# Performance work log

Measured on AMD Instinct MI355X. Metric: run time of the kernel, lower is better.

## Reference

```python
import jax, jax.numpy as jnp
import numpy as np

N = 4096; E = 32768; S = 64; V = 16; H0 = 64; H1 = 16; STEPS = 3
SQRT3 = float(np.sqrt(3.0))


def _tp(sx, vx, sy, vy):
    # full CG tensor product restricted to paths landing in 0e/1o
    # sx [n,m0], vx [n,m1,3], sy [n,k0], vy [n,k1,3]
    n = sx.shape[0]
    ss = (sx[:, :, None] * sy[:, None, :]).reshape(n, -1)              # 0e x 0e -> 0e
    dd = (jnp.einsum('nmi,nki->nmk', vx, vy) / SQRT3).reshape(n, -1)    # 1o . 1o -> 0e
    sv = (sx[:, :, None, None] * vy[:, None, :, :]).reshape(n, -1, 3)   # 0e x 1o -> 1o
    vs = (vx[:, :, None, :] * sy[:, None, :, None]).reshape(n, -1, 3)   # 1o x 0e -> 1o
    return jnp.concatenate([ss, dd], -1), jnp.concatenate([sv, vs], -2)


def _tpl_gate(sx, vx, sy, vy, ws, b, wv, n0):
    # TensorProductLinearGate: tensor_product -> Linear -> gate
    s_tp, v_tp = _tp(sx, vx, sy, vy)
    s = s_tp @ ws + b                                  # scalars + gate scalars
    v = jnp.einsum('ntd,tm->nmd', v_tp, wv)
    scal = jax.nn.gelu(s[:, :n0])
    gates = jax.nn.sigmoid(s[:, n0:])
    return scal, v * gates[:, :, None]


def _seg_mean(x, idx, n):
    s = jax.ops.segment_sum(x, idx, num_segments=n)
    c = jax.ops.segment_sum(jnp.ones((x.shape[0],), x.dtype), idx, num_segments=n)
    c = jnp.maximum(c, 1.0).reshape((n,) + (1,) * (x.ndim - 1))
    return s / c


def setup_inputs() -> dict:
    key = jax.random.key(0)
    ks = jax.random.split(key, 20)
    f32 = jnp.float32

    def w(k, shape):
        return jax.random.normal(k, shape, f32) / np.sqrt(shape[-2]).astype(np.float32)

    def bias(k, shape):
        return 0.1 * jax.random.normal(k, shape, f32)

    E1 = 2 * (S + V)          # 160: edge block0 TP width
    E2 = H0 + H1              # 80: edge blocks 1-2 TP width
    K0 = H0 + 1; K1 = H1 + 1  # message concat sh
    N0TP = S * K0 + V * K1    # 4432
    N1TP = S * K1 + V * K0    # 2128
    return {
        'node_s': jax.random.normal(ks[0], (N, S), f32),
        'node_v': jax.random.normal(ks[1], (N, V, 3), f32),
        'senders': jax.random.randint(ks[2], (E,), 0, N, jnp.int32),
        'receivers': jax.random.randint(ks[3], (E,), 0, N, jnp.int32),
        'e1_ws': w(ks[4], (STEPS, E1, H0 + H1)),
        'e1_b': bias(ks[5], (STEPS, H0 + H1)),
        'e1_wv': w(ks[6], (STEPS, E1, H1)),
        'e2_ws': w(ks[7], (STEPS, 2, E2, H0 + H1)),
        'e2_b': bias(ks[8], (STEPS, 2, H0 + H1)),
        'e2_wv': w(ks[9], (STEPS, 2, E2, H1)),
        'n_ws': w(ks[10], (STEPS, 3, N0TP, S + V)),
        'n_b': bias(ks[11], (STEPS, 3, S + V)),
        'n_wv': w(ks[12], (STEPS, 3, N1TP, V)),
        'l_ws': w(ks[13], (STEPS, S, S)),
        'l_b': bias(ks[14], (STEPS, S)),
        'l_wv': w(ks[15], (STEPS, V, V)),
    }


def reference(node_s, node_v, senders, receivers, e1_ws, e1_b, e1_wv,
              e2_ws, e2_b, e2_wv, n_ws, n_b, n_wv, l_ws, l_b, l_wv):
    norm = float(E - 1)
    for step in range(STEPS):
        s_i, v_i = node_s[senders], node_v[senders]
        s_j, v_j = node_s[receivers], node_v[receivers]
        r = v_i[:, 0] - v_j[:, 0]                    # slice_by_mul[:1] = positions
        rn = jnp.linalg.norm(r, axis=-1, keepdims=True)
        unit = r / jnp.maximum(rn, 1e-9)
        a_s = jnp.ones((E, 1), node_s.dtype)          # Y_0, component norm
        a_v = (SQRT3 * unit)[:, None, :]              # Y_1, component norm
        m_s = jnp.concatenate([s_i, s_j], -1)
        m_v = jnp.concatenate([v_i, v_j], -2)
        for blk in range(3):
            if blk == 0:
                ws, b, wv = e1_ws[step], e1_b[step], e1_wv[step]
            else:
                ws, b, wv = e2_ws[step, blk - 1], e2_b[step, blk - 1], e2_wv[step, blk - 1]
            m_s, m_v = _tpl_gate(m_s, m_v, a_s, a_v, ws, b, wv, H0)
        # ---- aggregate (segment_mean) + normalize_messages ----
        ms = _seg_mean(m_s, receivers, N) / norm
        mv = _seg_mean(m_v, receivers, N) / norm
        as_ = _seg_mean(a_s, receivers, N) / norm
        av = _seg_mean(a_v, receivers, N) / norm
        y_s = jnp.concatenate([ms, as_], -1)          # [N, H0+1]
        y_v = jnp.concatenate([mv, av], -2)           # [N, H1+1, 3]
        for blk in range(3):
            node_s, node_v = _tpl_gate(node_s, node_v, y_s, y_v,
                                       n_ws[step, blk], n_b[step, blk], n_wv[step, blk], S)
        # ---- final per-step Linear(irreps_in) ----
        node_s = node_s @ l_ws[step] + l_b[step]
        node_v = jnp.einsum('nmd,mk->nkd', node_v, l_wv[step])
    return jnp.concatenate([node_v.reshape(node_v.shape[0], -1), node_s], -1)
```

## Files before the change

### kernel.cpp

```cpp
#include <hip/hip_runtime.h>
#include <math.h>

constexpr int NND = 4096;
constexpr int EDG = 32768;
constexpr float SQRT3  = 1.7320508075688772f;
constexpr float ISQRT3 = 0.5773502691896258f;
constexpr float NORMI  = 1.0f / 32767.0f;

__device__ __forceinline__ float gelu_f(float x) {
    float x3 = x * x * x;
    return 0.5f * x * (1.0f + tanhf(0.7978845608028654f * (x + 0.044715f * x3)));
}
__device__ __forceinline__ float sigmoid_f(float x) {
    return 1.0f / (1.0f + expf(-x));
}

template<int NO4>
__device__ __forceinline__ void rank1(float* acc, float x, const float* w) {
#pragma unroll
    for (int u = 0; u < NO4; ++u) {
        const float4 q = *reinterpret_cast<const float4*>(w + 4 * u);
        acc[4*u+0] = fmaf(x, q.x, acc[4*u+0]);
        acc[4*u+1] = fmaf(x, q.y, acc[4*u+1]);
        acc[4*u+2] = fmaf(x, q.z, acc[4*u+2]);
        acc[4*u+3] = fmaf(x, q.w, acc[4*u+3]);
    }
}

__global__ __launch_bounds__(256)
void segnn_deg_kernel(const int* __restrict__ rcv, int* __restrict__ deg) {
    const int e = blockIdx.x * 256 + threadIdx.x;
    if (e < EDG) atomicAdd(deg + rcv[e], 1);
}

__global__ __launch_bounds__(1024)
void segnn_scan_kernel(const int* __restrict__ deg, int* __restrict__ off) {
    __shared__ int tots[1024];
    const int t = threadIdx.x;
    const int v0 = deg[4*t], v1 = deg[4*t+1], v2 = deg[4*t+2], v3 = deg[4*t+3];
    const int p1 = v0, p2 = p1 + v1, p3 = p2 + v2, p4 = p3 + v3;
    tots[t] = p4;
    __syncthreads();
    for (int d = 1; d < 1024; d <<= 1) {
        const int add = (t >= d) ? tots[t - d] : 0;
        __syncthreads();
        tots[t] += add;
        __syncthreads();
    }
    const int excl = t ? tots[t-1] : 0;
    off[4*t+0] = excl;
    off[4*t+1] = excl + p1;
    off[4*t+2] = excl + p2;
    off[4*t+3] = excl + p3;
    if (t == 1023) off[4096] = tots[1023];
}

__global__ __launch_bounds__(256)
void segnn_scatter_kernel(const int* __restrict__ rcv, const int* __restrict__ off,
                          int* __restrict__ cursor, int* __restrict__ elist) {
    const int e = blockIdx.x * 256 + threadIdx.x;
    if (e < EDG) {
        const int j = rcv[e];
        const int p = atomicAdd(cursor + j, 1);
        elist[off[j] + p] = e;
    }
}

template<int NSX, int NVX>
__device__ __forceinline__ void edge_gemm_phase(
    const int tid,
    const float* __restrict__ Ws, const float* __restrict__ Bs,
    const float* __restrict__ Wv,
    const float (*XT)[20], const float (*X2T)[20],
    float (*red)[16][8][6], float (*Cbuf)[96], float (*Cv)[48])
{
    const int cs   = tid & 15;
    const int rgl  = (tid >> 4) & 3;
    const int wvw  = tid >> 6;
    const int eg   = wvw & 1;
    const int kh   = wvw >> 1;
    const int lane = tid & 63;
    constexpr int KA = NSX + NVX;
    constexpr int CH = KA / 8;

    {
        float acc[8][6];
#pragma unroll
        for (int j = 0; j < 8; ++j)
#pragma unroll
            for (int c = 0; c < 6; ++c) acc[j][c] = 0.0f;
        const int r0 = (kh*4 + rgl) * CH;
#pragma unroll 2
        for (int rr = 0; rr < CH; ++rr) {
            const int r = r0 + rr;
            const float* wp = Ws + r*80 + cs;
            const float w0 = wp[0], w1 = wp[16], w2 = wp[32], w3 = wp[48], w4 = wp[64];
            const float w5 = (r < NSX) ? Wv[r*16 + cs] : 0.0f;
            const float4 xa = *reinterpret_cast<const float4*>(&XT[r][8*eg]);
            const float4 xb = *reinterpret_cast<const float4*>(&XT[r][8*eg+4]);
            const float xe[8] = { xa.x,xa.y,xa.z,xa.w, xb.x,xb.y,xb.z,xb.w };
#pragma unroll
            for (int j = 0; j < 8; ++j) {
                acc[j][0] = fmaf(xe[j], w0, acc[j][0]);
                acc[j][1] = fmaf(xe[j], w1, acc[j][1]);
                acc[j][2] = fmaf(xe[j], w2, acc[j][2]);
                acc[j][3] = fmaf(xe[j], w3, acc[j][3]);
                acc[j][4] = fmaf(xe[j], w4, acc[j][4]);
                acc[j][5] = fmaf(xe[j], w5, acc[j][5]);
            }
        }
#pragma unroll
        for (int j = 0; j < 8; ++j)
#pragma unroll
            for (int c = 0; c < 6; ++c) {
                float a = acc[j][c];
                a += __shfl_xor(a, 16);
                a += __shfl_xor(a, 32);
                acc[j][c] = a;
            }
        if (lane < 16) {
#pragma unroll
            for (int j = 0; j < 8; ++j)
#pragma unroll
                for (int c = 0; c < 6; ++c) red[wvw][lane][j][c] = acc[j][c];
        }
    }
    __syncthreads();
    for (int idx = tid; idx < 16*96; idx += 256) {
        const int e = idx / 96, col = idx - e*96;
        const int eg2 = e >> 3, j = e & 7;
        const int cs2 = col & 15, ci = col >> 4;
        float s = red[eg2][cs2][j][ci] + red[2+eg2][cs2][j][ci];
        if (col < 80) s += Bs[col];
        Cbuf[e][col] = s;
    }
    __syncthreads();

    {
        constexpr int CHB = NVX / 8;
        float av[8][3];
#pragma unroll
        for (int j = 0; j < 8; ++j) { av[j][0]=0.0f; av[j][1]=0.0f; av[j][2]=0.0f; }
        const int m0 = (kh*4 + rgl) * CHB;
#pragma unroll
        for (int mm = 0; mm < CHB; ++mm) {
            const int m = m0 + mm;
            const float w = Wv[(NSX + m)*16 + cs];
#pragma unroll
            for (int d = 0; d < 3; ++d) {
                const float4 xa = *reinterpret_cast<const float4*>(&X2T[d*NVX + m][8*eg]);
                const float4 xb = *reinterpret_cast<const float4*>(&X2T[d*NVX + m][8*eg+4]);
                const float xe[8] = { xa.x,xa.y,xa.z,xa.w, xb.x,xb.y,xb.z,xb.w };
#pragma unroll
                for (int j = 0; j < 8; ++j) av[j][d] = fmaf(xe[j], w, av[j][d]);
            }
        }
#pragma unroll
        for (int j = 0; j < 8; ++j)
#pragma unroll
            for (int d = 0; d < 3; ++d) {
                float a = av[j][d];
                a += __shfl_xor(a, 16);
                a += __shfl_xor(a, 32);
                av[j][d] = a;
            }
        if (lane < 16) {
#pragma unroll
            for (int j = 0; j < 8; ++j)
#pragma unroll
                for (int d = 0; d < 3; ++d) red[wvw][lane][j][d] = av[j][d];
        }
    }
    __syncthreads();
    for (int idx = tid; idx < 16*48; idx += 256) {
        const int e = idx / 48, q = idx - e*48;
        const int o = q / 3, d = q - 3*o;
        const int eg2 = e >> 3, j = e & 7;
        Cv[e][q] = red[eg2][o][j][d] + red[2+eg2][o][j][d];
    }
    __syncthreads();
}

__global__ __launch_bounds__(256, 3)
void segnn_edge_fused(const float* __restrict__ cs, const float* __restrict__ cv,
                      const int* __restrict__ snd, const int* __restrict__ rcv,
                      const float* __restrict__ W0s, const float* __restrict__ B0, const float* __restrict__ W0v,
                      const float* __restrict__ W1s, const float* __restrict__ B1, const float* __restrict__ W1v,
                      const float* __restrict__ W2s, const float* __restrict__ B2, const float* __restrict__ W2v,
                      float* __restrict__ msg) {
    __shared__ __align__(16) float XT[160][20];
    __shared__ __align__(16) float X2T[96][20];
    __shared__ float red[4][16][8][6];
    __shared__ float Cbuf[16][96];
    __shared__ float Cv[16][48];
    __shared__ float uu[16][4];
    __shared__ int   nd[16][2];

    const int tid = threadIdx.x;
    const int e0  = blockIdx.x * 16;

    if (tid < 16) { nd[tid][0] = snd[e0+tid]; nd[tid][1] = rcv[e0+tid]; }
    __syncthreads();
    for (int idx = tid; idx < 16*128; idx += 256) {
        const int e = idx >> 7, m = idx & 127;
        const int node = nd[e][m >> 6];
        XT[m][e] = cs[(size_t)node*64 + (m & 63)];
    }
    for (int idx = tid; idx < 16*96; idx += 256) {
        const int e = idx / 96, q = idx - e*96;
        const int part = q / 48, md = q - part*48;
        const int m = md / 3, d = md - m*3;
        const int node = nd[e][part];
        X2T[d*32 + part*16 + m][e] = cv[(size_t)node*48 + m*3 + d];
    }
    __syncthreads();
    if (tid < 16) {
        const float rx = X2T[0][tid]  - X2T[16][tid];
        const float ry = X2T[32][tid] - X2T[48][tid];
        const float rz = X2T[64][tid] - X2T[80][tid];
        const float rinv = 1.0f / fmaxf(sqrtf(rx*rx+ry*ry+rz*rz), 1e-9f);
        uu[tid][0] = rx*rinv; uu[tid][1] = ry*rinv; uu[tid][2] = rz*rinv;
    }
    __syncthreads();
    for (int idx = tid; idx < 16*32; idx += 256) {
        const int e = idx >> 5, mm = idx & 31;
        XT[128 + mm][e] = X2T[mm][e]*uu[e][0] + X2T[32+mm][e]*uu[e][1] + X2T[64+mm][e]*uu[e][2];
    }
    __syncthreads();

    edge_gemm_phase<128,32>(tid, W0s, B0, W0v, XT, X2T, red, Cbuf, Cv);
    for (int idx = tid; idx < 16*64; idx += 256) {
        const int e = idx >> 6, m = idx & 63;
        XT[m][e] = gelu_f(Cbuf[e][m]);
    }
    for (int idx = tid; idx < 16*16; idx += 256) {
        const int e = idx >> 4, o = idx & 15;
        const float g = sigmoid_f(Cbuf[e][64+o]);
        const float t = Cbuf[e][80+o] * SQRT3;
        float p = 0.0f;
#pragma unroll
        for (int d = 0; d < 3; ++d) {
            const float vd = fmaf(t, uu[e][d], Cv[e][o*3+d]) * g;
            X2T[d*16 + o][e] = vd;
            p = fmaf(vd, uu[e][d], p);
        }
        XT[64 + o][e] = p;
    }
    __syncthreads();

    edge_gemm_phase<64,16>(tid, W1s, B1, W1v, XT, X2T, red, Cbuf, Cv);
    for (int idx = tid; idx < 16*64; idx += 256) {
        const int e = idx >> 6, m = idx & 63;
        XT[m][e] = gelu_f(Cbuf[e][m]);
    }
    for (int idx = tid; idx < 16*16; idx += 256) {
        const int e = idx >> 4, o = idx & 15;
        const float g = sigmoid_f(Cbuf[e][64+o]);
        const float t = Cbuf[e][80+o] * SQRT3;
        float p = 0.0f;
#pragma unroll
        for (int d = 0; d < 3; ++d) {
            const float vd = fmaf(t, uu[e][d], Cv[e][o*3+d]) * g;
            X2T[d*16 + o][e] = vd;
            p = fmaf(vd, uu[e][d], p);
        }
        XT[64 + o][e] = p;
    }
    __syncthreads();

    edge_gemm_phase<64,16>(tid, W2s, B2, W2v, XT, X2T, red, Cbuf, Cv);
    for (int idx = tid; idx < 16*115; idx += 256) {
        const int e = idx / 115, f = idx - e*115;
        float vv;
        if (f < 64) {
            vv = gelu_f(Cbuf[e][f]);
        } else if (f < 112) {
            const int q = f - 64, o = q / 3, d = q - 3*o;
            const float g = sigmoid_f(Cbuf[e][64+o]);
            vv = fmaf(Cbuf[e][80+o] * SQRT3, uu[e][d], Cv[e][q]) * g;
        } else {
            vv = uu[e][f-112];
        }
        msg[(size_t)(e0+e)*116 + f] = vv;
    }
}

__global__ __launch_bounds__(128)
void segnn_gather_kernel(const float* __restrict__ msg, const int* __restrict__ off,
                         const int* __restrict__ elist,
                         float* __restrict__ y_s, float* __restrict__ y_v) {
    const int n = blockIdx.x, f = threadIdx.x;
    const int o0 = off[n], o1 = off[n+1];
    const int deg = o1 - o0;
    float acc = 0.0f;
    for (int p = o0; p < o1; ++p) {
        const int eid = elist[p];
        if (f < 115) acc += msg[(size_t)eid*116 + f];
    }
    const float inv = NORMI / (float)(deg > 0 ? deg : 1);
    if (f < 64)        y_s[(size_t)n*65 + f] = acc * inv;
    else if (f < 112)  y_v[(size_t)n*51 + (f-64)] = acc * inv;
    else if (f < 115)  y_v[(size_t)n*51 + 48 + (f-112)] = SQRT3 * acc * inv;
    else if (f == 115) y_s[(size_t)n*65 + 64] = deg ? NORMI : 0.0f;
}

__global__ __launch_bounds__(512, 4)
void segnn_node_kernel(const float* __restrict__ in_s, const float* __restrict__ in_v,
                       const float* __restrict__ y_s, const float* __restrict__ y_v,
                       const float* __restrict__ W,  const float* __restrict__ B,
                       const float* __restrict__ Wv,
                       float* __restrict__ out_s, float* __restrict__ out_v) {
    __shared__ __align__(16) float xsL[8*65];
    __shared__ __align__(16) float ysL[8*65];
    __shared__ __align__(16) float xvL[8*49];
    __shared__ __align__(16) float yvL[8*51];
    __shared__ __align__(16) float Xa[2][3072];
    __shared__ __align__(16) float red[8][16][40];
    __shared__ float finGG[8*16];

    const int tid  = threadIdx.x;
    const int lane = tid & 63;
    const int wv   = tid >> 6;
    const int nb0  = blockIdx.x * 8;

    for (int idx = tid; idx < 8*64; idx += 512) { const int n = idx >> 6, m = idx & 63; xsL[n*65+m] = in_s[(size_t)(nb0+n)*64 + m]; }
    for (int idx = tid; idx < 8*65; idx += 512) { const int n = idx / 65, k = idx - n*65; ysL[n*65+k] = y_s[(size_t)(nb0+n)*65 + k]; }
    for (int idx = tid; idx < 8*48; idx += 512) { const int n = idx / 48, m = idx - n*48; xvL[n*49+m] = in_v[(size_t)(nb0+n)*48 + m]; }
    for (int idx = tid; idx < 8*51; idx += 512) { const int n = idx / 51, m = idx - n*51; yvL[n*51+m] = y_v[(size_t)(nb0+n)*51 + m]; }
    __syncthreads();

    {
        const int cs = tid & 15;
        const int rowgrp = tid >> 4;

        float acc[8][5];
#pragma unroll
        for (int n = 0; n < 8; ++n)
#pragma unroll
            for (int c = 0; c < 5; ++c) acc[n][c] = 0.0f;

        auto genS = [&](int t, int b) {
            const int base = t * 128;
#pragma unroll
            for (int ii = 0; ii < 2; ++ii) {
                const int idx = tid + ii*512;
                const int rl = idx >> 3, n = idx & 7;
                const int r = base + rl;
                float val = 0.0f;
                if (r < 4160) {
                    const int m = r / 65, k = r - m*65;
                    val = xsL[n*65+m] * ysL[n*65+k];
                } else if (r < 4432) {
                    const int q = r - 4160;
                    const int m = q / 17, k = q - m*17;
                    val = (xvL[n*49+m*3+0]*yvL[n*51+k*3+0] +
                           xvL[n*49+m*3+1]*yvL[n*51+k*3+1] +
                           xvL[n*49+m*3+2]*yvL[n*51+k*3+2]) * ISQRT3;
                }
                Xa[b][idx] = val;
            }
        };

        genS(0, 0);
        __syncthreads();
        for (int t = 0; t < 35; ++t) {
            if (t + 1 < 35) genS(t + 1, (t + 1) & 1);
            const int base = t * 128;
            const float* Xb = &Xa[t & 1][0];
#pragma unroll
            for (int vv = 0; vv < 4; ++vv) {
                const int rl = rowgrp + 32*vv;
                const int r  = base + rl;
                const int wr = r < 4431 ? r : 4431;
                const float* wp = W + (size_t)wr * 80 + cs;
                const float w0 = wp[0], w1 = wp[16], w2 = wp[32], w3 = wp[48], w4_ = wp[64];
                const float4 xq0 = *reinterpret_cast<const float4*>(&Xb[rl*8]);
                const float4 xq1 = *reinterpret_cast<const float4*>(&Xb[rl*8+4]);
                const float xn[8] = { xq0.x, xq0.y, xq0.z, xq0.w, xq1.x, xq1.y, xq1.z, xq1.w };
#pragma unroll
                for (int n = 0; n < 8; ++n) {
                    acc[n][0] = fmaf(xn[n], w0,  acc[n][0]);
                    acc[n][1] = fmaf(xn[n], w1,  acc[n][1]);
                    acc[n][2] = fmaf(xn[n], w2,  acc[n][2]);
                    acc[n][3] = fmaf(xn[n], w3,  acc[n][3]);
                    acc[n][4] = fmaf(xn[n], w4_, acc[n][4]);
                }
            }
            __syncthreads();
        }

#pragma unroll
        for (int n = 0; n < 8; ++n)
#pragma unroll
            for (int c = 0; c < 5; ++c) {
                float a = acc[n][c];
                a += __shfl_xor(a, 16);
                a += __shfl_xor(a, 32);
                if (lane < 16) red[wv][lane][n*5+c] = a;
            }
        __syncthreads();
        for (int idx = tid; idx < 8*80; idx += 512) {
            const int n = idx / 80, col = idx - n*80;
            const int cs2 = col & 15, ci2 = col >> 4;
            float s = B[col];
#pragma unroll
            for (int w = 0; w < 8; ++w) s += red[w][cs2][n*5+ci2];
            if (col < 64) out_s[(size_t)(nb0+n)*64 + col] = gelu_f(s);
            else          finGG[n*16 + (col-64)] = s;
        }
    }

    {
        const int j4 = tid & 3;
        const int ngrp = (tid >> 2) & 1;
        const int rg = tid >> 3;

        float av[12][4];
#pragma unroll
        for (int a = 0; a < 12; ++a)
#pragma unroll
            for (int c = 0; c < 4; ++c) av[a][c] = 0.0f;

        auto genV = [&](int t, int b) {
            const int base = t * 128;
#pragma unroll
            for (int ii = 0; ii < 6; ++ii) {
                const int idx = tid + ii*512;
                const int rl = idx / 24, ar = idx - rl*24;
                const int n = ar / 3, d = ar - n*3;
                const int r = base + rl;
                float val = 0.0f;
                if (r < 1088) {
                    const int m = r / 17, k = r - m*17;
                    val = xsL[n*65+m] * yvL[n*51+k*3+d];
                } else if (r < 2128) {
                    const int q = r - 1088;
                    const int m = q / 65, k = q - m*65;
                    val = xvL[n*49+m*3+d] * ysL[n*65+k];
                }
                Xa[b][idx] = val;
            }
        };

        genV(0, 0);
        __syncthreads();
        for (int t = 0; t < 17; ++t) {
            if (t + 1 < 17) genV(t + 1, (t + 1) & 1);
            const int base = t * 128;
            const float* Xb = &Xa[t & 1][0];
#pragma unroll
            for (int vv = 0; vv < 2; ++vv) {
                const int rl = rg + 64*vv;
                const int r  = base + rl;
                const int wr = r < 2127 ? r : 2127;
                const float4 w4 = *reinterpret_cast<const float4*>(&Wv[(size_t)wr*16 + 4*j4]);
                const float4 xq0 = *reinterpret_cast<const float4*>(&Xb[rl*24 + 12*ngrp]);
                const float4 xq1 = *reinterpret_cast<const float4*>(&Xb[rl*24 + 12*ngrp + 4]);
                const float4 xq2 = *reinterpret_cast<const float4*>(&Xb[rl*24 + 12*ngrp + 8]);
                const float xr[12] = { xq0.x,xq0.y,xq0.z,xq0.w, xq1.x,xq1.y,xq1.z,xq1.w, xq2.x,xq2.y,xq2.z,xq2.w };
#pragma unroll
                for (int a = 0; a < 12; ++a) {
                    av[a][0] = fmaf(xr[a], w4.x, av[a][0]);
                    av[a][1] = fmaf(xr[a], w4.y, av[a][1]);
                    av[a][2] = fmaf(xr[a], w4.z, av[a][2]);
                    av[a][3] = fmaf(xr[a], w4.w, av[a][3]);
                }
            }
            __syncthreads();
        }

        float* redf = &red[0][0][0];
#pragma unroll
        for (int a = 0; a < 12; ++a)
#pragma unroll
            for (int c = 0; c < 4; ++c) {
                float x = av[a][c];
                x += __shfl_xor(x, 8);
                x += __shfl_xor(x, 16);
                x += __shfl_xor(x, 32);
                if (lane < 8) redf[wv*384 + lane*48 + a*4 + c] = x;
            }
        __syncthreads();
        for (int idx = tid; idx < 24*16; idx += 512) {
            const int ar = idx >> 4, j = idx & 15;
            const int n = ar / 3, d = ar - n*3;
            const int ng2 = ar / 12, a2 = ar - 12*ng2;
            const int jj4 = j >> 2, c2 = j & 3;
            float s = 0.0f;
#pragma unroll
            for (int w = 0; w < 8; ++w) s += redf[w*384 + (jj4 + 4*ng2)*48 + a2*4 + c2];
            out_v[(size_t)(nb0+n)*48 + j*3 + d] = s * sigmoid_f(finGG[n*16 + j]);
        }
    }
}

__global__ __launch_bounds__(256)
void segnn_linear_kernel(const float* __restrict__ in_s, const float* __restrict__ in_v,
                         const float* __restrict__ lws, const float* __restrict__ lb,
                         const float* __restrict__ lwv,
                         float* __restrict__ out_s, float* __restrict__ out_v,
                         float* __restrict__ out_cat) {
    const int idx = blockIdx.x * 256 + threadIdx.x;
    if (idx >= NND * 112) return;
    const int nidx = idx / 112, f = idx - nidx * 112;
    if (f < 48) {
        const int k = f / 3, d = f - 3*k;
        const float* vp = in_v + (size_t)nidx * 48 + d;
        float acc = 0.0f;
#pragma unroll
        for (int m = 0; m < 16; ++m) acc = fmaf(vp[m*3], lwv[m*16 + k], acc);
        if (out_cat) out_cat[(size_t)nidx*112 + f] = acc;
        else         out_v[(size_t)nidx*48 + f] = acc;
    } else {
        const int o = f - 48;
        const float* sp = in_s + (size_t)nidx * 64;
        float acc = lb[o];
#pragma unroll
        for (int m = 0; m < 64; ++m) acc = fmaf(sp[m], lws[m*64 + o], acc);
        if (out_cat) out_cat[(size_t)nidx*112 + f] = acc;
        else         out_s[(size_t)nidx*64 + o] = acc;
    }
}

extern "C" void kernel_launch(void* const* d_in, const int* in_sizes, int n_in,
                              void* d_out, int out_size, void* d_ws, size_t ws_size,
                              hipStream_t stream) {
    const float* in_s  = (const float*)d_in[0];
    const float* in_v  = (const float*)d_in[1];
    const int*   snd   = (const int*)  d_in[2];
    const int*   rcv   = (const int*)  d_in[3];
    const float* e1_ws = (const float*)d_in[4];
    const float* e1_b  = (const float*)d_in[5];
    const float* e1_wv = (const float*)d_in[6];
    const float* e2_ws = (const float*)d_in[7];
    const float* e2_b  = (const float*)d_in[8];
    const float* e2_wv = (const float*)d_in[9];
    const float* n_ws  = (const float*)d_in[10];
    const float* n_b   = (const float*)d_in[11];
    const float* n_wv  = (const float*)d_in[12];
    const float* l_ws  = (const float*)d_in[13];
    const float* l_b   = (const float*)d_in[14];
    const float* l_wv  = (const float*)d_in[15];

    float* ws    = (float*)d_ws;
    float* cur_s = ws;
    float* cur_v = cur_s + 262144;
    float* nxt_s = cur_v + 196608;
    float* nxt_v = nxt_s + 262144;
    float* y_s   = nxt_v + 196608;
    float* y_v   = y_s + 266240;
    float* msg   = y_v + 208896;
    int*   deg    = (int*)(msg + 3801088);
    int*   cursor = deg + 4096;
    int*   off    = cursor + 4096;
    int*   elist  = off + 4097;

    hipMemsetAsync(deg, 0, (size_t)8192 * sizeof(int), stream);
    hipMemcpyAsync(cur_s, in_s, (size_t)262144 * sizeof(float), hipMemcpyDeviceToDevice, stream);
    hipMemcpyAsync(cur_v, in_v, (size_t)196608 * sizeof(float), hipMemcpyDeviceToDevice, stream);
    segnn_deg_kernel<<<EDG/256, 256, 0, stream>>>(rcv, deg);
    segnn_scan_kernel<<<1, 1024, 0, stream>>>(deg, off);
    segnn_scatter_kernel<<<EDG/256, 256, 0, stream>>>(rcv, off, cursor, elist);

    for (int step = 0; step < 3; ++step) {
        segnn_edge_fused<<<EDG/16, 256, 0, stream>>>(cur_s, cur_v, snd, rcv,
            e1_ws + (size_t)step*160*80, e1_b + step*80, e1_wv + (size_t)step*160*16,
            e2_ws + (size_t)(step*2+0)*80*80, e2_b + (step*2+0)*80, e2_wv + (size_t)(step*2+0)*80*16,
            e2_ws + (size_t)(step*2+1)*80*80, e2_b + (step*2+1)*80, e2_wv + (size_t)(step*2+1)*80*16,
            msg);
        segnn_gather_kernel<<<NND, 128, 0, stream>>>(msg, off, elist, y_s, y_v);

        segnn_node_kernel<<<NND/8, 512, 0, stream>>>(cur_s, cur_v, y_s, y_v,
            n_ws + (size_t)(step*3+0)*4432*80, n_b + (step*3+0)*80, n_wv + (size_t)(step*3+0)*2128*16,
            nxt_s, nxt_v);
        segnn_node_kernel<<<NND/8, 512, 0, stream>>>(nxt_s, nxt_v, y_s, y_v,
            n_ws + (size_t)(step*3+1)*4432*80, n_b + (step*3+1)*80, n_wv + (size_t)(step*3+1)*2128*16,
            cur_s, cur_v);
        segnn_node_kernel<<<NND/8, 512, 0, stream>>>(cur_s, cur_v, y_s, y_v,
            n_ws + (size_t)(step*3+2)*4432*80, n_b + (step*3+2)*80, n_wv + (size_t)(step*3+2)*2128*16,
            nxt_s, nxt_v);

        segnn_linear_kernel<<<(NND*112 + 255)/256, 256, 0, stream>>>(nxt_s, nxt_v,
            l_ws + (size_t)step*64*64, l_b + step*64, l_wv + (size_t)step*16*16,
            cur_s, cur_v, (step == 2) ? (float*)d_out : nullptr);
    }
}
```

Measured before the change: 1.181 ms.

## Make edge kernel warp-independent and prefetch node-kernel weights into registers

The edge kernel now gives each 64-lane wave its own 8 edges with private shared buffers. Partial sums are reduced with shuffles and written directly, which removes the block-wide reduction buffers and most __syncthreads; each block handles 32 edges. The node kernel prefetches the next tile's weights into registers alongside the shared-memory generation and uses raw s_barrier with an lgkmcnt wait. Reduction buffers are padded against bank conflicts. Occupancy hints drop from 3 and 4 blocks per SM to 2, trading occupancy for register headroom, and the wave-private path relies on compiler barriers alone for ordering within a wave.

```diff
diff --git a/kernel.cpp b/kernel.cpp
--- a/kernel.cpp
+++ b/kernel.cpp
@@ -13,18 +13,6 @@
 }
 __device__ __forceinline__ float sigmoid_f(float x) {
     return 1.0f / (1.0f + expf(-x));
-}
-
-template<int NO4>
-__device__ __forceinline__ void rank1(float* acc, float x, const float* w) {
-#pragma unroll
-    for (int u = 0; u < NO4; ++u) {
-        const float4 q = *reinterpret_cast<const float4*>(w + 4 * u);
-        acc[4*u+0] = fmaf(x, q.x, acc[4*u+0]);
-        acc[4*u+1] = fmaf(x, q.y, acc[4*u+1]);
-        acc[4*u+2] = fmaf(x, q.z, acc[4*u+2]);
-        acc[4*u+3] = fmaf(x, q.w, acc[4*u+3]);
-    }
 }
 
 __global__ __launch_bounds__(256)
@@ -67,21 +55,15 @@
 }
 
 template<int NSX, int NVX>
-__device__ __forceinline__ void edge_gemm_phase(
-    const int tid,
+__device__ __forceinline__ void edge_phase_w(
+    const int lane,
     const float* __restrict__ Ws, const float* __restrict__ Bs,
     const float* __restrict__ Wv,
-    const float (*XT)[20], const float (*X2T)[20],
-    float (*red)[16][8][6], float (*Cbuf)[96], float (*Cv)[48])
+    float (*xt)[10], float (*x2)[10], float (*cb)[96], float (*cvv)[48])
 {
-    const int cs   = tid & 15;
-    const int rgl  = (tid >> 4) & 3;
-    const int wvw  = tid >> 6;
-    const int eg   = wvw & 1;
-    const int kh   = wvw >> 1;
-    const int lane = tid & 63;
+    const int cs = lane & 15, kg = lane >> 4;
     constexpr int KA = NSX + NVX;
-    constexpr int CH = KA / 8;
+    constexpr int CH = KA / 4;
 
     {
         float acc[8][6];
@@ -89,16 +71,18 @@
         for (int j = 0; j < 8; ++j)
 #pragma unroll
             for (int c = 0; c < 6; ++c) acc[j][c] = 0.0f;
-        const int r0 = (kh*4 + rgl) * CH;
-#pragma unroll 2
+        const int r0 = kg * CH;
+#pragma unroll 4
         for (int rr = 0; rr < CH; ++rr) {
             const int r = r0 + rr;
             const float* wp = Ws + r*80 + cs;
             const float w0 = wp[0], w1 = wp[16], w2 = wp[32], w3 = wp[48], w4 = wp[64];
             const float w5 = (r < NSX) ? Wv[r*16 + cs] : 0.0f;
-            const float4 xa = *reinterpret_cast<const float4*>(&XT[r][8*eg]);
-            const float4 xb = *reinterpret_cast<const float4*>(&XT[r][8*eg+4]);
-            const float xe[8] = { xa.x,xa.y,xa.z,xa.w, xb.x,xb.y,xb.z,xb.w };
+            const float2 xa = *reinterpret_cast<const float2*>(&xt[r][0]);
+            const float2 xb = *reinterpret_cast<const float2*>(&xt[r][2]);
+            const float2 xc = *reinterpret_cast<const float2*>(&xt[r][4]);
+            const float2 xd = *reinterpret_cast<const float2*>(&xt[r][6]);
+            const float xe[8] = { xa.x,xa.y, xb.x,xb.y, xc.x,xc.y, xd.x,xd.y };
 #pragma unroll
             for (int j = 0; j < 8; ++j) {
                 acc[j][0] = fmaf(xe[j], w0, acc[j][0]);
@@ -120,37 +104,31 @@
             }
         if (lane < 16) {
 #pragma unroll
-            for (int j = 0; j < 8; ++j)
-#pragma unroll
-                for (int c = 0; c < 6; ++c) red[wvw][lane][j][c] = acc[j][c];
-        }
-    }
-    __syncthreads();
-    for (int idx = tid; idx < 16*96; idx += 256) {
-        const int e = idx / 96, col = idx - e*96;
-        const int eg2 = e >> 3, j = e & 7;
-        const int cs2 = col & 15, ci = col >> 4;
-        float s = red[eg2][cs2][j][ci] + red[2+eg2][cs2][j][ci];
-        if (col < 80) s += Bs[col];
-        Cbuf[e][col] = s;
-    }
-    __syncthreads();
+            for (int j = 0; j < 8; ++j) {
+#pragma unroll
+                for (int c = 0; c < 5; ++c) cb[j][cs + 16*c] = acc[j][c] + Bs[cs + 16*c];
+                cb[j][80 + cs] = acc[j][5];
+            }
+        }
+    }
 
     {
-        constexpr int CHB = NVX / 8;
+        constexpr int CHB = NVX / 4;
         float av[8][3];
 #pragma unroll
         for (int j = 0; j < 8; ++j) { av[j][0]=0.0f; av[j][1]=0.0f; av[j][2]=0.0f; }
-        const int m0 = (kh*4 + rgl) * CHB;
+        const int m0 = kg * CHB;
 #pragma unroll
         for (int mm = 0; mm < CHB; ++mm) {
             const int m = m0 + mm;
             const float w = Wv[(NSX + m)*16 + cs];
 #pragma unroll
             for (int d = 0; d < 3; ++d) {
-                const float4 xa = *reinterpret_cast<const float4*>(&X2T[d*NVX + m][8*eg]);
-                const float4 xb = *reinterpret_cast<const float4*>(&X2T[d*NVX + m][8*eg+4]);
-                const float xe[8] = { xa.x,xa.y,xa.z,xa.w, xb.x,xb.y,xb.z,xb.w };
+                const float2 xa = *reinterpret_cast<const float2*>(&x2[d*NVX + m][0]);
+                const float2 xb = *reinterpret_cast<const float2*>(&x2[d*NVX + m][2]);
+                const float2 xc = *reinterpret_cast<const float2*>(&x2[d*NVX + m][4]);
+                const float2 xd = *reinterpret_cast<const float2*>(&x2[d*NVX + m][6]);
+                const float xe[8] = { xa.x,xa.y, xb.x,xb.y, xc.x,xc.y, xd.x,xd.y };
 #pragma unroll
                 for (int j = 0; j < 8; ++j) av[j][d] = fmaf(xe[j], w, av[j][d]);
             }
@@ -168,120 +146,130 @@
 #pragma unroll
             for (int j = 0; j < 8; ++j)
 #pragma unroll
-                for (int d = 0; d < 3; ++d) red[wvw][lane][j][d] = av[j][d];
-        }
-    }
-    __syncthreads();
-    for (int idx = tid; idx < 16*48; idx += 256) {
-        const int e = idx / 48, q = idx - e*48;
-        const int o = q / 3, d = q - 3*o;
-        const int eg2 = e >> 3, j = e & 7;
-        Cv[e][q] = red[eg2][o][j][d] + red[2+eg2][o][j][d];
-    }
-    __syncthreads();
-}
-
-__global__ __launch_bounds__(256, 3)
+                for (int d = 0; d < 3; ++d) cvv[j][cs*3 + d] = av[j][d];
+        }
+    }
+    asm volatile("" ::: "memory");
+}
+
+__global__ __launch_bounds__(256, 2)
 void segnn_edge_fused(const float* __restrict__ cs, const float* __restrict__ cv,
                       const int* __restrict__ snd, const int* __restrict__ rcv,
                       const float* __restrict__ W0s, const float* __restrict__ B0, const float* __restrict__ W0v,
                       const float* __restrict__ W1s, const float* __restrict__ B1, const float* __restrict__ W1v,
                       const float* __restrict__ W2s, const float* __restrict__ B2, const float* __restrict__ W2v,
                       float* __restrict__ msg) {
-    __shared__ __align__(16) float XT[160][20];
-    __shared__ __align__(16) float X2T[96][20];
-    __shared__ float red[4][16][8][6];
-    __shared__ float Cbuf[16][96];
-    __shared__ float Cv[16][48];
-    __shared__ float uu[16][4];
-    __shared__ int   nd[16][2];
-
-    const int tid = threadIdx.x;
-    const int e0  = blockIdx.x * 16;
-
-    if (tid < 16) { nd[tid][0] = snd[e0+tid]; nd[tid][1] = rcv[e0+tid]; }
-    __syncthreads();
-    for (int idx = tid; idx < 16*128; idx += 256) {
-        const int e = idx >> 7, m = idx & 127;
-        const int node = nd[e][m >> 6];
-        XT[m][e] = cs[(size_t)node*64 + (m & 63)];
-    }
-    for (int idx = tid; idx < 16*96; idx += 256) {
-        const int e = idx / 96, q = idx - e*96;
-        const int part = q / 48, md = q - part*48;
-        const int m = md / 3, d = md - m*3;
-        const int node = nd[e][part];
-        X2T[d*32 + part*16 + m][e] = cv[(size_t)node*48 + m*3 + d];
-    }
-    __syncthreads();
-    if (tid < 16) {
-        const float rx = X2T[0][tid]  - X2T[16][tid];
-        const float ry = X2T[32][tid] - X2T[48][tid];
-        const float rz = X2T[64][tid] - X2T[80][tid];
+    __shared__ __align__(16) float XT [4][160][10];
+    __shared__ __align__(16) float X2T[4][96][10];
+    __shared__ __align__(16) float Cb [4][8][96];
+    __shared__ __align__(16) float Cv [4][8][48];
+    __shared__ float UU [4][8][4];
+
+    const int tid  = threadIdx.x;
+    const int w    = tid >> 6;
+    const int lane = tid & 63;
+    const int e0   = blockIdx.x * 32 + w * 8;
+
+    float (*xt)[10]  = XT[w];
+    float (*x2)[10]  = X2T[w];
+    float (*cb)[96]  = Cb[w];
+    float (*cvv)[48] = Cv[w];
+    float (*uuw)[4]  = UU[w];
+
+#pragma unroll
+    for (int it = 0; it < 16; ++it) {
+        const int e = it >> 1, half = it & 1;
+        const int node = (half ? rcv : snd)[e0 + e];
+        xt[half*64 + lane][e] = cs[(size_t)node*64 + lane];
+    }
+#pragma unroll
+    for (int it = 0; it < 16; ++it) {
+        const int e = it >> 1, half = it & 1;
+        if (lane < 48) {
+            const int node = (half ? rcv : snd)[e0 + e];
+            const int m = lane / 3, d = lane - 3*m;
+            x2[d*32 + half*16 + m][e] = cv[(size_t)node*48 + lane];
+        }
+    }
+    asm volatile("" ::: "memory");
+    if (lane < 8) {
+        const float rx = x2[0][lane]  - x2[16][lane];
+        const float ry = x2[32][lane] - x2[48][lane];
+        const float rz = x2[64][lane] - x2[80][lane];
         const float rinv = 1.0f / fmaxf(sqrtf(rx*rx+ry*ry+rz*rz), 1e-9f);
-        uu[tid][0] = rx*rinv; uu[tid][1] = ry*rinv; uu[tid][2] = rz*rinv;
-    }
-    __syncthreads();
-    for (int idx = tid; idx < 16*32; idx += 256) {
+        uuw[lane][0] = rx*rinv; uuw[lane][1] = ry*rinv; uuw[lane][2] = rz*rinv;
+    }
+    asm volatile("" ::: "memory");
+#pragma unroll
+    for (int it = 0; it < 4; ++it) {
+        const int idx = it*64 + lane;
         const int e = idx >> 5, mm = idx & 31;
-        XT[128 + mm][e] = X2T[mm][e]*uu[e][0] + X2T[32+mm][e]*uu[e][1] + X2T[64+mm][e]*uu[e][2];
-    }
-    __syncthreads();
-
-    edge_gemm_phase<128,32>(tid, W0s, B0, W0v, XT, X2T, red, Cbuf, Cv);
-    for (int idx = tid; idx < 16*64; idx += 256) {
-        const int e = idx >> 6, m = idx & 63;
-        XT[m][e] = gelu_f(Cbuf[e][m]);
-    }
-    for (int idx = tid; idx < 16*16; idx += 256) {
+        xt[128 + mm][e] = x2[mm][e]*uuw[e][0] + x2[32+mm][e]*uuw[e][1] + x2[64+mm][e]*uuw[e][2];
+    }
+    asm volatile("" ::: "memory");
+
+    edge_phase_w<128,32>(lane, W0s, B0, W0v, xt, x2, cb, cvv);
+#pragma unroll
+    for (int it = 0; it < 8; ++it) {
+        xt[lane][it] = gelu_f(cb[it][lane]);
+    }
+#pragma unroll
+    for (int it = 0; it < 2; ++it) {
+        const int idx = it*64 + lane;
         const int e = idx >> 4, o = idx & 15;
-        const float g = sigmoid_f(Cbuf[e][64+o]);
-        const float t = Cbuf[e][80+o] * SQRT3;
+        const float g = sigmoid_f(cb[e][64+o]);
+        const float t = cb[e][80+o] * SQRT3;
         float p = 0.0f;
 #pragma unroll
         for (int d = 0; d < 3; ++d) {
-            const float vd = fmaf(t, uu[e][d], Cv[e][o*3+d]) * g;
-            X2T[d*16 + o][e] = vd;
-            p = fmaf(vd, uu[e][d], p);
-        }
-        XT[64 + o][e] = p;
-    }
-    __syncthreads();
-
-    edge_gemm_phase<64,16>(tid, W1s, B1, W1v, XT, X2T, red, Cbuf, Cv);
-    for (int idx = tid; idx < 16*64; idx += 256) {
-        const int e = idx >> 6, m = idx & 63;
-        XT[m][e] = gelu_f(Cbuf[e][m]);
-    }
-    for (int idx = tid; idx < 16*16; idx += 256) {
+            const float vd = fmaf(t, uuw[e][d], cvv[e][o*3+d]) * g;
+            x2[d*16 + o][e] = vd;
+            p = fmaf(vd, uuw[e][d], p);
+        }
+        xt[64 + o][e] = p;
+    }
+    asm volatile("" ::: "memory");
+
+    edge_phase_w<64,16>(lane, W1s, B1, W1v, xt, x2, cb, cvv);
+#pragma unroll
+    for (int it = 0; it < 8; ++it) {
+        xt[lane][it] = gelu_f(cb[it][lane]);
+    }
+#pragma unroll
+    for (int it = 0; it < 2; ++it) {
+        const int idx = it*64 + lane;
         const int e = idx >> 4, o = idx & 15;
-        const float g = sigmoid_f(Cbuf[e][64+o]);
-        const float t = Cbuf[e][80+o] * SQRT3;
+        const float g = sigmoid_f(cb[e][64+o]);
+        const float t = cb[e][80+o] * SQRT3;
         float p = 0.0f;
 #pragma unroll
         for (int d = 0; d < 3; ++d) {
-            const float vd = fmaf(t, uu[e][d], Cv[e][o*3+d]) * g;
-            X2T[d*16 + o][e] = vd;
-            p = fmaf(vd, uu[e][d], p);
-        }
-        XT[64 + o][e] = p;
-    }
-    __syncthreads();
-
-    edge_gemm_phase<64,16>(tid, W2s, B2, W2v, XT, X2T, red, Cbuf, Cv);
-    for (int idx = tid; idx < 16*115; idx += 256) {
-        const int e = idx / 115, f = idx - e*115;
-        float vv;
-        if (f < 64) {
-            vv = gelu_f(Cbuf[e][f]);
-        } else if (f < 112) {
-            const int q = f - 64, o = q / 3, d = q - 3*o;
-            const float g = sigmoid_f(Cbuf[e][64+o]);
-            vv = fmaf(Cbuf[e][80+o] * SQRT3, uu[e][d], Cv[e][q]) * g;
-        } else {
-            vv = uu[e][f-112];
-        }
-        msg[(size_t)(e0+e)*116 + f] = vv;
+            const float vd = fmaf(t, uuw[e][d], cvv[e][o*3+d]) * g;
+            x2[d*16 + o][e] = vd;
+            p = fmaf(vd, uuw[e][d], p);
+        }
+        xt[64 + o][e] = p;
+    }
+    asm volatile("" ::: "memory");
+
+    edge_phase_w<64,16>(lane, W2s, B2, W2v, xt, x2, cb, cvv);
+#pragma unroll
+    for (int it = 0; it < 15; ++it) {
+        const int idx = it*64 + lane;
+        if (idx < 920) {
+            const int e = idx / 115, f = idx - 115*e;
+            float vv;
+            if (f < 64) {
+                vv = gelu_f(cb[e][f]);
+            } else if (f < 112) {
+                const int q = f - 64, o = q / 3, d = q - 3*o;
+                const float g = sigmoid_f(cb[e][64+o]);
+                vv = fmaf(cb[e][80+o] * SQRT3, uuw[e][d], cvv[e][q]) * g;
+            } else {
+                vv = uuw[e][f-112];
+            }
+            msg[(size_t)(e0+e)*116 + f] = vv;
+        }
     }
 }
 
@@ -304,7 +292,7 @@
     else if (f == 115) y_s[(size_t)n*65 + 64] = deg ? NORMI : 0.0f;
 }
 
-__global__ __launch_bounds__(512, 4)
+__global__ __launch_bounds__(512, 2)
 void segnn_node_kernel(const float* __restrict__ in_s, const float* __restrict__ in_v,
                        const float* __restrict__ y_s, const float* __restrict__ y_v,
                        const float* __restrict__ W,  const float* __restrict__ B,
@@ -315,7 +303,7 @@
     __shared__ __align__(16) float xvL[8*49];
     __shared__ __align__(16) float yvL[8*51];
     __shared__ __align__(16) float Xa[2][3072];
-    __shared__ __align__(16) float red[8][16][40];
+    __shared__ __align__(16) float red[8][16][41];
     __shared__ float finGG[8*16];
 
     const int tid  = threadIdx.x;
@@ -360,33 +348,49 @@
                 Xa[b][idx] = val;
             }
         };
-
-        genS(0, 0);
-        __syncthreads();
-        for (int t = 0; t < 35; ++t) {
-            if (t + 1 < 35) genS(t + 1, (t + 1) & 1);
+        auto loadW = [&](int t, float wreg[4][5]) {
             const int base = t * 128;
-            const float* Xb = &Xa[t & 1][0];
-#pragma unroll
-            for (int vv = 0; vv < 4; ++vv) {
-                const int rl = rowgrp + 32*vv;
-                const int r  = base + rl;
+#pragma unroll
+            for (int v2 = 0; v2 < 4; ++v2) {
+                const int r = base + rowgrp + 32*v2;
                 const int wr = r < 4431 ? r : 4431;
                 const float* wp = W + (size_t)wr * 80 + cs;
-                const float w0 = wp[0], w1 = wp[16], w2 = wp[32], w3 = wp[48], w4_ = wp[64];
+                wreg[v2][0] = wp[0];  wreg[v2][1] = wp[16]; wreg[v2][2] = wp[32];
+                wreg[v2][3] = wp[48]; wreg[v2][4] = wp[64];
+            }
+        };
+
+        float wc[4][5], wn[4][5];
+        loadW(0, wc);
+        genS(0, 0);
+        asm volatile("s_waitcnt lgkmcnt(0)" ::: "memory");
+        __builtin_amdgcn_s_barrier();
+        asm volatile("" ::: "memory");
+        for (int t = 0; t < 35; ++t) {
+            if (t + 1 < 35) { loadW(t + 1, wn); genS(t + 1, (t + 1) & 1); }
+            const float* Xb = &Xa[t & 1][0];
+#pragma unroll
+            for (int v2 = 0; v2 < 4; ++v2) {
+                const int rl = rowgrp + 32*v2;
                 const float4 xq0 = *reinterpret_cast<const float4*>(&Xb[rl*8]);
                 const float4 xq1 = *reinterpret_cast<const float4*>(&Xb[rl*8+4]);
                 const float xn[8] = { xq0.x, xq0.y, xq0.z, xq0.w, xq1.x, xq1.y, xq1.z, xq1.w };
 #pragma unroll
                 for (int n = 0; n < 8; ++n) {
-                    acc[n][0] = fmaf(xn[n], w0,  acc[n][0]);
-                    acc[n][1] = fmaf(xn[n], w1,  acc[n][1]);
-                    acc[n][2] = fmaf(xn[n], w2,  acc[n][2]);
-                    acc[n][3] = fmaf(xn[n], w3,  acc[n][3]);
-                    acc[n][4] = fmaf(xn[n], w4_, acc[n][4]);
+                    acc[n][0] = fmaf(xn[n], wc[v2][0], acc[n][0]);
+                    acc[n][1] = fmaf(xn[n], wc[v2][1], acc[n][1]);
+                    acc[n][2] = fmaf(xn[n], wc[v2][2], acc[n][2]);
+                    acc[n][3] = fmaf(xn[n], wc[v2][3], acc[n][3]);
+                    acc[n][4] = fmaf(xn[n], wc[v2][4], acc[n][4]);
                 }
             }
-            __syncthreads();
+            asm volatile("s_waitcnt lgkmcnt(0)" ::: "memory");
+            __builtin_amdgcn_s_barrier();
+            asm volatile("" ::: "memory");
+#pragma unroll
+            for (int v2 = 0; v2 < 4; ++v2)
+#pragma unroll
+                for (int c = 0; c < 5; ++c) wc[v2][c] = wn[v2][c];
         }
 
 #pragma unroll
@@ -404,10 +408,11 @@
             const int cs2 = col & 15, ci2 = col >> 4;
             float s = B[col];
 #pragma unroll
-            for (int w = 0; w < 8; ++w) s += red[w][cs2][n*5+ci2];
+            for (int ww = 0; ww < 8; ++ww) s += red[ww][cs2][n*5+ci2];
             if (col < 64) out_s[(size_t)(nb0+n)*64 + col] = gelu_f(s);
             else          finGG[n*16 + (col-64)] = s;
         }
+        __syncthreads();
     }
 
     {
@@ -441,19 +446,28 @@
                 Xa[b][idx] = val;
             }
         };
-
+        auto loadWv = [&](int t, float4 wreg[2]) {
+#pragma unroll
+            for (int v2 = 0; v2 < 2; ++v2) {
+                const int r = t*128 + rg + 64*v2;
+                const int wr = r < 2127 ? r : 2127;
+                wreg[v2] = *reinterpret_cast<const float4*>(&Wv[(size_t)wr*16 + 4*j4]);
+            }
+        };
+
+        float4 wqc[2], wqn[2];
+        loadWv(0, wqc);
         genV(0, 0);
-        __syncthreads();
+        asm volatile("s_waitcnt lgkmcnt(0)" ::: "memory");
+        __builtin_amdgcn_s_barrier();
+        asm volatile("" ::: "memory");
         for (int t = 0; t < 17; ++t) {
-            if (t + 1 < 17) genV(t + 1, (t + 1) & 1);
-            const int base = t * 128;
+            if (t + 1 < 17) { loadWv(t + 1, wqn); genV(t + 1, (t + 1) & 1); }
             const float* Xb = &Xa[t & 1][0];
 #pragma unroll
-            for (int vv = 0; vv < 2; ++vv) {
-                const int rl = rg + 64*vv;
-                const int r  = base + rl;
-                const int wr = r < 2127 ? r : 2127;
-                const float4 w4 = *reinterpret_cast<const float4*>(&Wv[(size_t)wr*16 + 4*j4]);
+            for (int v2 = 0; v2 < 2; ++v2) {
+                const int rl = rg + 64*v2;
+                const float4 w4 = wqc[v2];
                 const float4 xq0 = *reinterpret_cast<const float4*>(&Xb[rl*24 + 12*ngrp]);
                 const float4 xq1 = *reinterpret_cast<const float4*>(&Xb[rl*24 + 12*ngrp + 4]);
                 const float4 xq2 = *reinterpret_cast<const float4*>(&Xb[rl*24 + 12*ngrp + 8]);
@@ -466,7 +480,10 @@
                     av[a][3] = fmaf(xr[a], w4.w, av[a][3]);
                 }
             }
-            __syncthreads();
+            asm volatile("s_waitcnt lgkmcnt(0)" ::: "memory");
+            __builtin_amdgcn_s_barrier();
+            asm volatile("" ::: "memory");
+            wqc[0] = wqn[0]; wqc[1] = wqn[1];
         }
 
         float* redf = &red[0][0][0];
@@ -478,7 +495,7 @@
                 x += __shfl_xor(x, 8);
                 x += __shfl_xor(x, 16);
                 x += __shfl_xor(x, 32);
-                if (lane < 8) redf[wv*384 + lane*48 + a*4 + c] = x;
+                if (lane < 8) redf[wv*392 + lane*49 + a*4 + c] = x;
             }
         __syncthreads();
         for (int idx = tid; idx < 24*16; idx += 512) {
@@ -488,7 +505,7 @@
             const int jj4 = j >> 2, c2 = j & 3;
             float s = 0.0f;
 #pragma unroll
-            for (int w = 0; w < 8; ++w) s += redf[w*384 + (jj4 + 4*ng2)*48 + a2*4 + c2];
+            for (int ww = 0; ww < 8; ++ww) s += redf[ww*392 + (jj4 + 4*ng2)*49 + a2*4 + c2];
             out_v[(size_t)(nb0+n)*48 + j*3 + d] = s * sigmoid_f(finGG[n*16 + j]);
         }
     }
@@ -563,7 +580,7 @@
     segnn_scatter_kernel<<<EDG/256, 256, 0, stream>>>(rcv, off, cursor, elist);
 
     for (int step = 0; step < 3; ++step) {
-        segnn_edge_fused<<<EDG/16, 256, 0, stream>>>(cur_s, cur_v, snd, rcv,
+        segnn_edge_fused<<<EDG/32, 256, 0, stream>>>(cur_s, cur_v, snd, rcv,
             e1_ws + (size_t)step*160*80, e1_b + step*80, e1_wv + (size_t)step*160*16,
             e2_ws + (size_t)(step*2+0)*80*80, e2_b + (step*2+0)*80, e2_wv + (size_t)(step*2+0)*80*16,
             e2_ws + (size_t)(step*2+1)*80*80, e2_b + (step*2+1)*80, e2_wv + (size_t)(step*2+1)*80*16,
```

Result: slower. 1.301 ms (+10.2%).
